# Kernel tuning notes

Hardware: AMD Instinct MI355X
Metric: run time of the kernel (lower is better)

## Reference

```python
import jax, jax.numpy as jnp
import numpy as np

C = 256      # dim_in == dim_out (residual add requires it)
H = 96
W = 96
Z = 16       # number of (isWithin, dist) pairs
MAXL = 8


def setup_inputs() -> dict:
    key = jax.random.key(0)
    ks = jax.random.split(key, 8)
    x = jax.random.normal(ks[0], (1, C, H, W), jnp.float32)
    # 1x1 convs without bias == channel matmuls with weight [out_ch, in_ch]
    Wq = jax.random.normal(ks[1], (C, C), jnp.float32) / np.sqrt(C).astype(np.float32)
    Wk = jax.random.normal(ks[2], (C, C), jnp.float32) / np.sqrt(C).astype(np.float32)
    Wv = jax.random.normal(ks[3], (C, C), jnp.float32) / np.sqrt(C).astype(np.float32)
    embd = jax.random.normal(ks[4], (2, 2 * MAXL + 1, C), jnp.float32)  # N(0,1) as in torch
    Wproj = jax.random.normal(ks[5], (C, C + 1), jnp.float32) / np.sqrt(C + 1).astype(np.float32)
    dist = jax.random.randint(ks[6], (Z,), 0, 2 * MAXL + 1) - MAXL      # in [-maxl, maxl]
    isWithin = jax.random.randint(ks[7], (Z,), 0, 2)                     # in {0, 1}
    return {"x": x, "Wq": Wq, "Wk": Wk, "Wv": Wv, "embd": embd,
            "Wproj": Wproj, "dist": dist, "isWithin": isWithin}


def reference(x, Wq, Wk, Wv, embd, Wproj, dist, isWithin):
    b, c, hh, ww = x.shape
    n = hh * ww
    maxl = (embd.shape[1] - 1) // 2
    xf = x.reshape(b, c, n)                                  # [b, c, n]
    q = jnp.einsum('oc,bcn->bon', Wq, xf)                    # 1x1 conv == channel matmul
    k = jnp.einsum('oc,bcn->bon', Wk, xf)
    v = jnp.einsum('oc,bcn->bon', Wv, xf)
    # full (unscaled) attention over spatial tokens, softmax along q axis
    att = jax.nn.softmax(jnp.einsum('bck,bcq->bkq', k, q), axis=-1)  # [b, n, n]
    Y = jnp.einsum('bkq,bck->bcq', att, v)                   # [b, c, n]
    out = Y.reshape(b, c, hh, ww) + x                        # residual
    # relative-distance embedding gather: [z, c]
    rel = embd[isWithin, dist + maxl]
    pos = jnp.einsum('zc,bcn->bzn', rel, xf)                 # [b, z, n] (u=1 folded)
    pos = pos.reshape(b * pos.shape[1], 1, hh, ww)           # [(b z), 1, hh, ww]
    z = pos.shape[0]
    out_rep = jnp.tile(out, (z, 1, 1, 1))                    # [z, c, hh, ww] (b == 1)
    cat = jnp.concatenate([out_rep, pos], axis=1)            # [z, c+1, hh, ww]
    return jnp.einsum('oc,zchw->zohw', Wproj, cat)           # final 1x1 conv
```

## Files before the change

kernel.cpp:

```cpp
#include <hip/hip_runtime.h>
#include <hip/hip_bf16.h>

typedef __bf16 bf8 __attribute__((ext_vector_type(8)));
typedef __bf16 bfx4 __attribute__((ext_vector_type(4)));
typedef float f4 __attribute__((ext_vector_type(4)));

#define NTOK 9216
#define CDIM 256
#define LOG2E 1.44269504f
#define PSHIFT 32.0f

__device__ inline bf8 ldfrag(const __bf16* p, int ld) {
  int l = threadIdx.x & 63;
  return *reinterpret_cast<const bf8*>(p + (l & 15) * ld + ((l >> 4) << 3));
}
__device__ inline f4 mfma16(bf8 a, bf8 b, f4 c) {
  return __builtin_amdgcn_mfma_f32_16x16x32_bf16(a, b, c, 0, 0, 0);
}
__device__ inline void gl2lds(const __bf16* g, __bf16* l) {
  __builtin_amdgcn_global_load_lds(
      (const __attribute__((address_space(1))) void*)g,
      (__attribute__((address_space(3))) void*)l, 16, 0, 0);
}

template <int EPI>
__global__ __launch_bounds__(256) void gemm128(const __bf16* __restrict__ A, int lda,
                                               const __bf16* __restrict__ Bt, int ldb,
                                               void* __restrict__ Cv, int ldc, int K,
                                               const float* __restrict__ aux0,
                                               const float* __restrict__ aux1) {
  __shared__ __bf16 As[128 * 32];
  __shared__ __bf16 Bs[128 * 32];
  const int tid = threadIdx.x;
  const int w = tid >> 6, lane = tid & 63;
  const int lc = lane & 15, quad = lane >> 4;
  const int m0 = blockIdx.x * 128, n0 = blockIdx.y * 128;
  const int wm = (w & 1) << 6, wn = (w >> 1) << 6;
  const int r0 = (w * 2) * 16 + (lane >> 2);
  const int cg = (lane & 3) * 8;
  const __bf16* gA0 = A + (size_t)(m0 + r0) * lda + cg;
  const __bf16* gA1 = A + (size_t)(m0 + r0 + 16) * lda + cg;
  const __bf16* gB0 = Bt + (size_t)(n0 + r0) * ldb + cg;
  const __bf16* gB1 = Bt + (size_t)(n0 + r0 + 16) * ldb + cg;
  __bf16* lA0 = As + (w * 2) * 512;
  __bf16* lA1 = As + (w * 2 + 1) * 512;
  __bf16* lB0 = Bs + (w * 2) * 512;
  __bf16* lB1 = Bs + (w * 2 + 1) * 512;

  f4 acc[4][4] = {};
  for (int kk = 0; kk < K; kk += 32) {
    __syncthreads();
    gl2lds(gA0 + kk, lA0);
    gl2lds(gA1 + kk, lA1);
    gl2lds(gB0 + kk, lB0);
    gl2lds(gB1 + kk, lB1);
    __syncthreads();
    bf8 af[4], bfr[4];
    for (int i = 0; i < 4; i++) af[i] = ldfrag(As + (wm + 16 * i) * 32, 32);
    for (int j = 0; j < 4; j++) bfr[j] = ldfrag(Bs + (wn + 16 * j) * 32, 32);
    for (int i = 0; i < 4; i++)
      for (int j = 0; j < 4; j++) acc[i][j] = mfma16(af[i], bfr[j], acc[i][j]);
  }
  if (EPI == 4) {
    float* outp = (float*)Cv;
    const int z0 = blockIdx.z * 4;
    for (int i = 0; i < 4; i++)
      for (int r = 0; r < 4; r++) {
        int o = m0 + wm + 16 * i + quad * 4 + r;
        float wo = aux1[o];
        for (int j = 0; j < 4; j++) {
          int n = n0 + wn + 16 * j + lc;
          float b = acc[i][j][r];
          for (int z = z0; z < z0 + 4; z++)
            outp[((size_t)z * 256 + o) * NTOK + n] =
                b + wo * aux0[(size_t)z * NTOK + n];
        }
      }
  } else {
    for (int i = 0; i < 4; i++)
      for (int j = 0; j < 4; j++)
        for (int r = 0; r < 4; r++) {
          size_t idx = (size_t)(m0 + wm + 16 * i + quad * 4 + r) * ldc +
                       (n0 + wn + 16 * j + lc);
          ((__bf16*)Cv)[idx] = (__bf16)acc[i][j][r];
        }
  }
}

__global__ __launch_bounds__(256) void sgemm_kernel(const __bf16* __restrict__ Kt,
                                                    const __bf16* __restrict__ Qt,
                                                    __bf16* __restrict__ Pp,
                                                    float* __restrict__ Pd) {
  __shared__ __bf16 As[2][128 * 32];
  __shared__ __bf16 Bs[2][128 * 32];
  const int tid = threadIdx.x;
  const int w = tid >> 6, lane = tid & 63;
  const int lc = lane & 15, quad = lane >> 4;
  const int m0 = blockIdx.x * 128;
  const int n0 = blockIdx.y * 128;
  const int wm = (w & 1) << 6, wn = (w >> 1) << 6;
  const int r0 = w * 32 + (lane >> 2);
  const int cg = (lane & 3) * 8;
  const __bf16* gA0 = Kt + (size_t)(m0 + r0) * 512 + cg;
  const __bf16* gA1 = Kt + (size_t)(m0 + r0 + 16) * 512 + cg;
  const __bf16* gB0 = Qt + (size_t)(n0 + r0) * 512 + cg;
  const __bf16* gB1 = Qt + (size_t)(n0 + r0 + 16) * 512 + cg;
  const int la = w * 1024;

  for (int p = 0; p < 2; p++) {
    gl2lds(gA0 + p * 32, &As[p][la]);
    gl2lds(gA1 + p * 32, &As[p][la + 512]);
    gl2lds(gB0 + p * 32, &Bs[p][la]);
    gl2lds(gB1 + p * 32, &Bs[p][la + 512]);
  }

  f4 acc[4][4] = {};
  for (int s = 0; s < 8; s++) {
    const int cur = s & 1;
    asm volatile("s_waitcnt vmcnt(4)" ::: "memory");
    __builtin_amdgcn_sched_barrier(0);
    __builtin_amdgcn_s_barrier();
    __builtin_amdgcn_sched_barrier(0);
    bf8 af[4], bfr[4];
    for (int i = 0; i < 4; i++) af[i] = ldfrag(&As[cur][(wm + 16 * i) * 32], 32);
    for (int j = 0; j < 4; j++) bfr[j] = ldfrag(&Bs[cur][(wn + 16 * j) * 32], 32);
    __builtin_amdgcn_s_setprio(1);
    for (int i = 0; i < 4; i++)
      for (int j = 0; j < 4; j++) acc[i][j] = mfma16(af[i], bfr[j], acc[i][j]);
    __builtin_amdgcn_s_setprio(0);
    __builtin_amdgcn_sched_barrier(0);
    __builtin_amdgcn_s_barrier();
    __builtin_amdgcn_sched_barrier(0);
    int sp = (s + 2 < 8) ? s + 2 : 7;
    gl2lds(gA0 + sp * 32, &As[cur][la]);
    gl2lds(gA1 + sp * 32, &As[cur][la + 512]);
    gl2lds(gB0 + sp * 32, &Bs[cur][la]);
    gl2lds(gB1 + sp * 32, &Bs[cur][la + 512]);
  }

  float dsum[4][4];
  for (int i = 0; i < 4; i++)
    for (int r = 0; r < 4; r++) dsum[i][r] = 0.f;
  for (int j = 0; j < 4; j++) {
    int q = n0 + wn + 16 * j + lc;
    for (int i = 0; i < 4; i++) {
      int ktb = m0 + wm + 16 * i;
      int c2 = ((i & 1) << 1) | (quad >> 1);
      bfx4 pk;
      for (int r = 0; r < 4; r++) {
        float e = exp2f(acc[i][j][r] - PSHIFT);
        dsum[i][r] += e;
        pk[r] = (__bf16)e;
      }
      __bf16* dst = Pp + ((size_t)(ktb >> 5) * NTOK + q) * 32 +
                    ((c2 ^ (lc & 3)) << 3) + ((quad & 1) << 2);
      *reinterpret_cast<bfx4*>(dst) = pk;
    }
  }
  for (int i = 0; i < 4; i++)
    for (int r = 0; r < 4; r++) {
      float d = dsum[i][r];
      d += __shfl_xor(d, 1);
      d += __shfl_xor(d, 2);
      d += __shfl_xor(d, 4);
      d += __shfl_xor(d, 8);
      dsum[i][r] = d;
    }
  if (lc == 0) {
    int mb = blockIdx.y * 2 + (w >> 1);
    for (int i = 0; i < 4; i++)
      for (int r = 0; r < 4; r++) {
        int kt = m0 + wm + 16 * i + quad * 4 + r;
        Pd[(size_t)kt * 144 + mb] = dsum[i][r];
      }
  }
}

__global__ __launch_bounds__(256) void prep_kernel(
    const float* Wq, const float* Wk, const float* Wv, const float* embd,
    const float* Wproj, const int* dist, const int* isWithin,
    __bf16* Wqkb, __bf16* Wvb, __bf16* Wpb, float* wl, __bf16* rel) {
  int tid = blockIdx.x * 256 + threadIdx.x;
  if (tid < 65536) {
    Wqkb[tid] = (__bf16)(Wq[tid] * LOG2E);
    Wqkb[65536 + tid] = (__bf16)Wk[tid];
    Wvb[tid] = (__bf16)Wv[tid];
    int o = tid >> 8, c = tid & 255;
    Wpb[tid] = (__bf16)Wproj[o * 257 + c];
    if (c == 0) wl[o] = Wproj[o * 257 + 256];
  }
  if (tid < 16 * 256) {
    int z = tid >> 8, c = tid & 255;
    rel[tid] = (__bf16)embd[(isWithin[z] * 17 + dist[z] + 8) * 256 + c];
  }
}

__global__ __launch_bounds__(256) void transpose_kernel(const float* x, __bf16* Xt) {
  __shared__ __bf16 tile[32][33];
  int n0 = blockIdx.x * 32;
  int c0 = blockIdx.y * 32;
  int tx = threadIdx.x & 31, ty = threadIdx.x >> 5;
  for (int i = 0; i < 32; i += 8)
    tile[ty + i][tx] = (__bf16)x[(c0 + ty + i) * NTOK + n0 + tx];
  __syncthreads();
  for (int i = 0; i < 32; i += 8)
    Xt[(n0 + ty + i) * CDIM + c0 + tx] = tile[tx][ty + i];
}

__global__ __launch_bounds__(256) void gemm_pos(const __bf16* rel, const __bf16* Xt,
                                                float* pos) {
  int n0 = blockIdx.x * 64 + (threadIdx.x >> 6) * 16;
  f4 acc = {};
  for (int ks = 0; ks < 256; ks += 32) {
    bf8 a = ldfrag(rel + ks, 256);
    bf8 b = ldfrag(Xt + (size_t)n0 * 256 + ks, 256);
    acc = mfma16(a, b, acc);
  }
  int l = threadIdx.x & 63, lc = l & 15, quad = l >> 4;
  for (int r = 0; r < 4; r++)
    pos[(quad * 4 + r) * NTOK + n0 + lc] = acc[r];
}

__global__ __launch_bounds__(256) void combine_stats(const float* __restrict__ Pd,
                                                     float* dinv) {
  int kt = blockIdx.x * 4 + (threadIdx.x >> 6);
  int lane = threadIdx.x & 63;
  const float* pd = Pd + (size_t)kt * 144;
  float d = pd[lane] + pd[lane + 64] + ((lane < 16) ? pd[lane + 128] : 0.f);
  for (int off = 1; off < 64; off <<= 1) d += __shfl_xor(d, off);
  if (lane == 0) dinv[kt] = 1.0f / d;
}

__global__ __launch_bounds__(256) void vscale_kernel(const __bf16* __restrict__ V,
                                                     const float* __restrict__ dinv,
                                                     __bf16* __restrict__ Vs) {
  size_t off = ((size_t)blockIdx.x * 256 + threadIdx.x) * 8;
  bf8 v = *reinterpret_cast<const bf8*>(V + off);
  int c = (int)(off / NTOK);
  int kt = (int)(off % NTOK);
  f4 dl = *reinterpret_cast<const f4*>(dinv + kt);
  f4 dh = *reinterpret_cast<const f4*>(dinv + kt + 4);
  bf8 o;
  for (int j = 0; j < 4; j++) o[j] = (__bf16)((float)v[j] * dl[j]);
  for (int j = 0; j < 4; j++) o[4 + j] = (__bf16)((float)v[4 + j] * dh[j]);
  int c2 = (kt >> 3) & 3;
  size_t dst = (size_t)c * NTOK + (kt & ~31) + (((c2 ^ (c & 3))) << 3);
  *reinterpret_cast<bf8*>(Vs + dst) = o;
}

template <int NSTEP>
__global__ __launch_bounds__(256) void pv_kernel(const __bf16* __restrict__ P,
                                                 const __bf16* __restrict__ Vp,
                                                 float* __restrict__ Ypart) {
  __shared__ __bf16 As[2][64 * 32];
  __shared__ __bf16 Bs[2][256 * 32];
  const int tid = threadIdx.x;
  const int w = tid >> 6, lane = tid & 63;
  const int lc = lane & 15, quad = lane >> 4;
  const int q0 = blockIdx.x * 64;
  const int z = blockIdx.y;
  const int wn = w << 6;
  const int sb0 = z * NSTEP;
  const __bf16* gA = P + ((size_t)sb0 * NTOK + q0) * 32 + w * 512 + lane * 8;
  const size_t aStride = (size_t)NTOK * 32;
  const __bf16* gB = Vp + (size_t)(w * 64 + (lane >> 2)) * NTOK + sb0 * 32 +
                     ((lane & 3) << 3);

  for (int p = 0; p < 2; p++) {
    gl2lds(gA + (size_t)p * aStride, &As[p][w * 512]);
    for (int u = 0; u < 4; u++)
      gl2lds(gB + (size_t)(16 * u) * NTOK + p * 32, &Bs[p][(w * 64 + 16 * u) * 32]);
  }

  f4 acc[4][4] = {};
  const int swz = (quad ^ (lc & 3)) << 3;
  for (int s = 0; s < NSTEP; s++) {
    const int cur = s & 1;
    asm volatile("s_waitcnt vmcnt(5)" ::: "memory");
    __builtin_amdgcn_sched_barrier(0);
    __builtin_amdgcn_s_barrier();
    __builtin_amdgcn_sched_barrier(0);
    bf8 af[4], bfr[4];
    for (int i = 0; i < 4; i++)
      af[i] = *reinterpret_cast<const bf8*>(&As[cur][(16 * i + lc) * 32 + swz]);
    for (int j = 0; j < 4; j++)
      bfr[j] = *reinterpret_cast<const bf8*>(&Bs[cur][(wn + 16 * j + lc) * 32 + swz]);
    __builtin_amdgcn_s_setprio(1);
    for (int i = 0; i < 4; i++)
      for (int j = 0; j < 4; j++) acc[i][j] = mfma16(af[i], bfr[j], acc[i][j]);
    __builtin_amdgcn_s_setprio(0);
    __builtin_amdgcn_sched_barrier(0);
    __builtin_amdgcn_s_barrier();
    __builtin_amdgcn_sched_barrier(0);
    int sp = (s + 2 < NSTEP) ? s + 2 : NSTEP - 1;
    gl2lds(gA + (size_t)sp * aStride, &As[cur][w * 512]);
    for (int u = 0; u < 4; u++)
      gl2lds(gB + (size_t)(16 * u) * NTOK + sp * 32, &Bs[cur][(w * 64 + 16 * u) * 32]);
  }

  float* Yp = Ypart + (size_t)z * NTOK * 256;
  for (int i = 0; i < 4; i++)
    for (int j = 0; j < 4; j++)
      for (int r = 0; r < 4; r++)
        Yp[(size_t)(q0 + 16 * i + quad * 4 + r) * 256 + wn + 16 * j + lc] =
            acc[i][j][r];
}

__global__ __launch_bounds__(256) void combine_y_kernel(const float* __restrict__ Ypart,
                                                        const __bf16* __restrict__ Xt,
                                                        __bf16* outT, int zp) {
  int i = blockIdx.x * 256 + threadIdx.x;
  f4 y = {};
  for (int z = 0; z < zp; z++) {
    f4 p = reinterpret_cast<const f4*>(Ypart + (size_t)z * NTOK * 256)[i];
    for (int t = 0; t < 4; t++) y[t] += p[t];
  }
  bfx4 xv = reinterpret_cast<const bfx4*>(Xt)[i];
  bfx4 o;
  for (int t = 0; t < 4; t++) o[t] = (__bf16)(y[t] + (float)xv[t]);
  reinterpret_cast<bfx4*>(outT)[i] = o;
}

extern "C" void kernel_launch(void* const* d_in, const int* in_sizes, int n_in,
                              void* d_out, int out_size, void* d_ws, size_t ws_size,
                              hipStream_t stream) {
  const float* x = (const float*)d_in[0];
  const float* Wq = (const float*)d_in[1];
  const float* Wk = (const float*)d_in[2];
  const float* Wv = (const float*)d_in[3];
  const float* embd = (const float*)d_in[4];
  const float* Wproj = (const float*)d_in[5];
  const int* dist = (const int*)d_in[6];
  const int* isW = (const int*)d_in[7];
  float* out = (float*)d_out;

  char* w8 = (char*)d_ws;
  __bf16* Xt = (__bf16*)(w8 + 0);
  __bf16* QKt = (__bf16*)(w8 + 4718592);
  __bf16* V = (__bf16*)(w8 + 14155776);
  __bf16* Wqkb = (__bf16*)(w8 + 18874368);
  __bf16* Wvb = (__bf16*)(w8 + 19136512);
  __bf16* Wpb = (__bf16*)(w8 + 19267584);
  __bf16* rel = (__bf16*)(w8 + 19398656);
  float* wl = (float*)(w8 + 19406848);
  float* pos = (float*)(w8 + 19407872);
  float* dinv = (float*)(w8 + 20034560);
  __bf16* Vs = (__bf16*)(w8 + 20971520);
  const size_t sOff = 29508608;
  __bf16* P = (__bf16*)(w8 + sOff);
  float* Pd = (float*)(w8 + sOff + 171966464);
  const size_t ypOff = sOff + 171966464 + 5308416;
  float* Ypart = (float*)(w8 + ypOff);
  __bf16* outT = (__bf16*)(w8 + sOff);

  static const int ZPS[] = {6, 4, 3, 2, 1};
  int zp = 1;
  for (int i = 0; i < 5; i++)
    if (ypOff + (size_t)ZPS[i] * 9437184 <= ws_size) { zp = ZPS[i]; break; }

  prep_kernel<<<256, 256, 0, stream>>>(Wq, Wk, Wv, embd, Wproj, dist, isW,
                                       Wqkb, Wvb, Wpb, wl, rel);
  transpose_kernel<<<dim3(288, 8), 256, 0, stream>>>(x, Xt);
  gemm128<1><<<dim3(72, 4), 256, 0, stream>>>(Xt, 256, Wqkb, 256, QKt, 512, 256,
                                              nullptr, nullptr);
  gemm128<1><<<dim3(2, 72), 256, 0, stream>>>(Wvb, 256, Xt, 256, V, NTOK, 256,
                                              nullptr, nullptr);
  gemm_pos<<<144, 256, 0, stream>>>(rel, Xt, pos);
  sgemm_kernel<<<dim3(72, 72), 256, 0, stream>>>(QKt + 256, QKt, P, Pd);
  combine_stats<<<2304, 256, 0, stream>>>(Pd, dinv);
  vscale_kernel<<<1152, 256, 0, stream>>>(V, dinv, Vs);
  switch (zp) {
    case 6: pv_kernel<48><<<dim3(144, 6), 256, 0, stream>>>(P, Vs, Ypart); break;
    case 4: pv_kernel<72><<<dim3(144, 4), 256, 0, stream>>>(P, Vs, Ypart); break;
    case 3: pv_kernel<96><<<dim3(144, 3), 256, 0, stream>>>(P, Vs, Ypart); break;
    case 2: pv_kernel<144><<<dim3(144, 2), 256, 0, stream>>>(P, Vs, Ypart); break;
    default: pv_kernel<288><<<dim3(144, 1), 256, 0, stream>>>(P, Vs, Ypart); break;
  }
  combine_y_kernel<<<2304, 256, 0, stream>>>(Ypart, Xt, outT, zp);
  gemm128<4><<<dim3(2, 72, 4), 256, 0, stream>>>(Wpb, 256, outT, 256, out, NTOK, 256,
                                                 pos, wl);
}
```

Before: 391.3 us.

## Double-buffer gemm128 loads and stream P fragments directly to registers in pv_kernel

gemm128 moves from a single LDS buffer with two syncthreads per k-step to a two-stage double-buffered async global-to-LDS pipeline with a vmcnt wait, setprio around the MFMAs, and a prefetch distance of two. pv_kernel drops the LDS staging of the P tile and loads the A fragments straight from global memory into registers, double-buffered through two register sets and a manually unrolled step macro. It also adds a launch-bounds occupancy hint. The aim is to hide global load latency and cut LDS traffic and barriers, at the cost of more registers and relying on the vmcnt counts being correct.

New measurement: 389.5 us. No clear change (-0.5%).

```diff
diff --git a/kernel.cpp b/kernel.cpp
--- a/kernel.cpp
+++ b/kernel.cpp
@@ -29,8 +29,8 @@
                                                void* __restrict__ Cv, int ldc, int K,
                                                const float* __restrict__ aux0,
                                                const float* __restrict__ aux1) {
-  __shared__ __bf16 As[128 * 32];
-  __shared__ __bf16 Bs[128 * 32];
+  __shared__ __bf16 As[2][128 * 32];
+  __shared__ __bf16 Bs[2][128 * 32];
   const int tid = threadIdx.x;
   const int w = tid >> 6, lane = tid & 63;
   const int lc = lane & 15, quad = lane >> 4;
@@ -42,25 +42,41 @@
   const __bf16* gA1 = A + (size_t)(m0 + r0 + 16) * lda + cg;
   const __bf16* gB0 = Bt + (size_t)(n0 + r0) * ldb + cg;
   const __bf16* gB1 = Bt + (size_t)(n0 + r0 + 16) * ldb + cg;
-  __bf16* lA0 = As + (w * 2) * 512;
-  __bf16* lA1 = As + (w * 2 + 1) * 512;
-  __bf16* lB0 = Bs + (w * 2) * 512;
-  __bf16* lB1 = Bs + (w * 2 + 1) * 512;
+  const int la = w * 1024;
+
+  for (int p = 0; p < 2; p++) {
+    gl2lds(gA0 + p * 32, &As[p][la]);
+    gl2lds(gA1 + p * 32, &As[p][la + 512]);
+    gl2lds(gB0 + p * 32, &Bs[p][la]);
+    gl2lds(gB1 + p * 32, &Bs[p][la + 512]);
+  }
 
   f4 acc[4][4] = {};
-  for (int kk = 0; kk < K; kk += 32) {
-    __syncthreads();
-    gl2lds(gA0 + kk, lA0);
-    gl2lds(gA1 + kk, lA1);
-    gl2lds(gB0 + kk, lB0);
-    gl2lds(gB1 + kk, lB1);
-    __syncthreads();
+  const int nst = K / 32;
+  for (int s = 0; s < nst; s++) {
+    const int cur = s & 1;
+    asm volatile("s_waitcnt vmcnt(4)" ::: "memory");
+    __builtin_amdgcn_sched_barrier(0);
+    __builtin_amdgcn_s_barrier();
+    __builtin_amdgcn_sched_barrier(0);
     bf8 af[4], bfr[4];
-    for (int i = 0; i < 4; i++) af[i] = ldfrag(As + (wm + 16 * i) * 32, 32);
-    for (int j = 0; j < 4; j++) bfr[j] = ldfrag(Bs + (wn + 16 * j) * 32, 32);
+    for (int i = 0; i < 4; i++) af[i] = ldfrag(&As[cur][(wm + 16 * i) * 32], 32);
+    for (int j = 0; j < 4; j++) bfr[j] = ldfrag(&Bs[cur][(wn + 16 * j) * 32], 32);
+    __builtin_amdgcn_s_setprio(1);
     for (int i = 0; i < 4; i++)
       for (int j = 0; j < 4; j++) acc[i][j] = mfma16(af[i], bfr[j], acc[i][j]);
-  }
+    __builtin_amdgcn_s_setprio(0);
+    __builtin_amdgcn_sched_barrier(0);
+    __builtin_amdgcn_s_barrier();
+    __builtin_amdgcn_sched_barrier(0);
+    int sp = (s + 2 < nst) ? s + 2 : nst - 1;
+    gl2lds(gA0 + sp * 32, &As[cur][la]);
+    gl2lds(gA1 + sp * 32, &As[cur][la + 512]);
+    gl2lds(gB0 + sp * 32, &Bs[cur][la]);
+    gl2lds(gB1 + sp * 32, &Bs[cur][la + 512]);
+  }
+  asm volatile("s_waitcnt vmcnt(0)" ::: "memory");
+
   if (EPI == 4) {
     float* outp = (float*)Cv;
     const int z0 = blockIdx.z * 4;
@@ -249,10 +265,9 @@
 }
 
 template <int NSTEP>
-__global__ __launch_bounds__(256) void pv_kernel(const __bf16* __restrict__ P,
-                                                 const __bf16* __restrict__ Vp,
-                                                 float* __restrict__ Ypart) {
-  __shared__ __bf16 As[2][64 * 32];
+__global__ __launch_bounds__(256, 4) void pv_kernel(const __bf16* __restrict__ P,
+                                                    const __bf16* __restrict__ Vp,
+                                                    float* __restrict__ Ypart) {
   __shared__ __bf16 Bs[2][256 * 32];
   const int tid = threadIdx.x;
   const int w = tid >> 6, lane = tid & 63;
@@ -261,42 +276,63 @@
   const int z = blockIdx.y;
   const int wn = w << 6;
   const int sb0 = z * NSTEP;
-  const __bf16* gA = P + ((size_t)sb0 * NTOK + q0) * 32 + w * 512 + lane * 8;
+  const int swz = (quad ^ (lc & 3)) << 3;
+  const __bf16* gAr = P + ((size_t)sb0 * NTOK + q0 + lc) * 32 + swz;
   const size_t aStride = (size_t)NTOK * 32;
   const __bf16* gB = Vp + (size_t)(w * 64 + (lane >> 2)) * NTOK + sb0 * 32 +
                      ((lane & 3) << 3);
 
-  for (int p = 0; p < 2; p++) {
-    gl2lds(gA + (size_t)p * aStride, &As[p][w * 512]);
-    for (int u = 0; u < 4; u++)
-      gl2lds(gB + (size_t)(16 * u) * NTOK + p * 32, &Bs[p][(w * 64 + 16 * u) * 32]);
-  }
+  bf8 afA[4], afB[4];
+  for (int u = 0; u < 4; u++)
+    gl2lds(gB + (size_t)(16 * u) * NTOK, &Bs[0][(w * 64 + 16 * u) * 32]);
+  __builtin_amdgcn_sched_barrier(0);
+#pragma unroll
+  for (int i = 0; i < 4; i++)
+    afA[i] = *reinterpret_cast<const bf8*>(gAr + i * 512);
+  __builtin_amdgcn_sched_barrier(0);
+  for (int u = 0; u < 4; u++)
+    gl2lds(gB + (size_t)(16 * u) * NTOK + 32, &Bs[1][(w * 64 + 16 * u) * 32]);
+  __builtin_amdgcn_sched_barrier(0);
+#pragma unroll
+  for (int i = 0; i < 4; i++)
+    afB[i] = *reinterpret_cast<const bf8*>(gAr + aStride + i * 512);
+  __builtin_amdgcn_sched_barrier(0);
 
   f4 acc[4][4] = {};
-  const int swz = (quad ^ (lc & 3)) << 3;
-  for (int s = 0; s < NSTEP; s++) {
-    const int cur = s & 1;
-    asm volatile("s_waitcnt vmcnt(5)" ::: "memory");
-    __builtin_amdgcn_sched_barrier(0);
-    __builtin_amdgcn_s_barrier();
-    __builtin_amdgcn_sched_barrier(0);
-    bf8 af[4], bfr[4];
-    for (int i = 0; i < 4; i++)
-      af[i] = *reinterpret_cast<const bf8*>(&As[cur][(16 * i + lc) * 32 + swz]);
-    for (int j = 0; j < 4; j++)
-      bfr[j] = *reinterpret_cast<const bf8*>(&Bs[cur][(wn + 16 * j + lc) * 32 + swz]);
-    __builtin_amdgcn_s_setprio(1);
-    for (int i = 0; i < 4; i++)
-      for (int j = 0; j < 4; j++) acc[i][j] = mfma16(af[i], bfr[j], acc[i][j]);
-    __builtin_amdgcn_s_setprio(0);
-    __builtin_amdgcn_sched_barrier(0);
-    __builtin_amdgcn_s_barrier();
-    __builtin_amdgcn_sched_barrier(0);
-    int sp = (s + 2 < NSTEP) ? s + 2 : NSTEP - 1;
-    gl2lds(gA + (size_t)sp * aStride, &As[cur][w * 512]);
-    for (int u = 0; u < 4; u++)
-      gl2lds(gB + (size_t)(16 * u) * NTOK + sp * 32, &Bs[cur][(w * 64 + 16 * u) * 32]);
-  }
+
+#define PV_STEP(s, CUR, AFU)                                                   \
+  {                                                                            \
+    asm volatile("s_waitcnt vmcnt(8)" ::: "memory");                           \
+    __builtin_amdgcn_sched_barrier(0);                                         \
+    __builtin_amdgcn_s_barrier();                                              \
+    __builtin_amdgcn_sched_barrier(0);                                         \
+    bf8 bfr[4];                                                                \
+    for (int j = 0; j < 4; j++)                                                \
+      bfr[j] = *reinterpret_cast<const bf8*>(                                  \
+          &Bs[CUR][(wn + 16 * j + lc) * 32 + swz]);                            \
+    __builtin_amdgcn_s_setprio(1);                                             \
+    for (int i = 0; i < 4; i++)                                                \
+      for (int j = 0; j < 4; j++)                                              \
+        acc[i][j] = mfma16(AFU[i], bfr[j], acc[i][j]);                         \
+    __builtin_amdgcn_s_setprio(0);                                             \
+    __builtin_amdgcn_sched_barrier(0);                                         \
+    __builtin_amdgcn_s_barrier();                                              \
+    __builtin_amdgcn_sched_barrier(0);                                         \
+    int sp = ((s) + 2 < NSTEP) ? (s) + 2 : NSTEP - 1;                          \
+    for (int u = 0; u < 4; u++)                                                \
+      gl2lds(gB + (size_t)(16 * u) * NTOK + sp * 32,                           \
+             &Bs[CUR][(w * 64 + 16 * u) * 32]);                                \
+    __builtin_amdgcn_sched_barrier(0);                                         \
+    _Pragma("unroll") for (int i = 0; i < 4; i++) AFU[i] =                     \
+        *reinterpret_cast<const bf8*>(gAr + (size_t)sp * aStride + i * 512);   \
+    __builtin_amdgcn_sched_barrier(0);                                         \
+  }
+
+  for (int s = 0; s < NSTEP; s += 2) {
+    PV_STEP(s, 0, afA);
+    PV_STEP(s + 1, 1, afB);
+  }
+#undef PV_STEP
 
   float* Yp = Ypart + (size_t)z * NTOK * 256;
   for (int i = 0; i < 4; i++)
```
